# Kernel optimization log

Hardware: AMD Instinct MI355X
Metric: run time of the kernel (lower is better)

Reference implementation:

```python
import jax, jax.numpy as jnp
import numpy as np

DIM = 64
NUM_HEADS = 4
SIGMA_RATIO = 1.0


def setup_inputs() -> dict:
    key = jax.random.key(0)
    ks = jax.random.split(key, 10)
    d = DIM
    s = 0.02
    return {
        "x": jax.random.normal(ks[0], (2, d, 64, 64), dtype=jnp.float32),
        "qkv_w": jax.random.normal(ks[1], (3 * d, d), dtype=jnp.float32) * s,
        "qkv_b": jnp.zeros((3 * d,), dtype=jnp.float32),
        "proj_w": jax.random.normal(ks[2], (d, d), dtype=jnp.float32) * s,
        "proj_b": jnp.zeros((d,), dtype=jnp.float32),
        "g1_w": jax.random.normal(ks[3], (16, 1), dtype=jnp.float32) * 0.5,
        "g1_b": jnp.zeros((16,), dtype=jnp.float32),
        "g2_w": jax.random.normal(ks[4], (NUM_HEADS, 16), dtype=jnp.float32) * 0.5,
        "g2_b": jnp.zeros((NUM_HEADS,), dtype=jnp.float32),
    }


def reference(x, qkv_w, qkv_b, proj_w, proj_b, g1_w, g1_b, g2_w, g2_b):
    B, C, H, W = x.shape
    nh = NUM_HEADS
    hd = C // nh
    N = H * W
    scale = hd ** -0.5

    # edge strength |x[i]-x[i-1]| summed over channels, replicate-padded
    diff_h = jnp.abs(x[:, :, :, 1:] - x[:, :, :, :-1]).sum(axis=1)  # [B,H,W-1]
    diff_v = jnp.abs(x[:, :, 1:, :] - x[:, :, :-1, :]).sum(axis=1)  # [B,H-1,W]
    edge_h = jnp.pad(diff_h, ((0, 0), (0, 0), (0, 1)), mode="edge")
    edge_v = jnp.pad(diff_v, ((0, 0), (0, 1), (0, 0)), mode="edge")
    es = (edge_h + edge_v)[..., None]  # [B,H,W,1]

    # gate MLP: Linear(1,16) -> GELU(exact) -> Linear(16,nh) -> sigmoid
    h1 = jax.nn.gelu(es @ g1_w.T + g1_b, approximate=False)
    gate = jax.nn.sigmoid(h1 @ g2_w.T + g2_b)  # [B,H,W,nh]

    x_seq = x.transpose(0, 2, 3, 1).reshape(B, N, C)
    qkv = (x_seq @ qkv_w.T + qkv_b).reshape(B, N, 3, nh, hd)
    qkv = qkv.transpose(2, 0, 3, 1, 4)  # [3,B,nh,N,hd]
    q, k, v = qkv[0], qkv[1], qkv[2]

    attn = jax.nn.softmax(jnp.einsum("bhnd,bhmd->bhnm", q, k) * scale, axis=-1)

    gate_sender = gate.reshape(B, N, nh).transpose(0, 2, 1)  # [B,nh,N]
    gate_sender = (1.0 - gate_sender * SIGMA_RATIO * 0.1)[..., None]  # [B,nh,N,1]
    attn = attn * gate_sender
    attn = attn / (attn.sum(axis=-1, keepdims=True) + 1e-8)

    out = jnp.einsum("bhnm,bhmd->bnhd", attn, v).reshape(B, N, C)
    out = out @ proj_w.T + proj_b
    return out.reshape(B, H, W, C).transpose(0, 3, 1, 2)
```

## Files before the change

kernel.cpp:

```cpp
#include <hip/hip_runtime.h>
#include <cstdint>


namespace {
constexpr int B  = 2;
constexpr int C  = 64;
constexpr int NH = 4;
constexpr int HD = 16;
constexpr int N  = 4096;
constexpr int MSA = 4;
constexpr int MT  = 256;
constexpr int VROW  = 2 * MT + 16;
constexpr int KSZ   = MT * 32;
constexpr int BUFSZ = KSZ + HD * VROW;

constexpr size_t QKV1     = (size_t)B * NH * N * HD;
constexpr size_t KB_OFF   = QKV1;
constexpr size_t VT_OFF   = 2 * QKV1;
constexpr size_t PO_OFF_U = 3 * QKV1;
constexpr size_t PO_SZ    = (size_t)B * NH * MSA * N * HD;
constexpr size_t PL_OFF_F = (PO_OFF_U + PO_SZ) / 2;
constexpr float QSCALE = 0.36067376022224085f;
}

typedef short bf16x8 __attribute__((ext_vector_type(8)));
typedef float f32x16 __attribute__((ext_vector_type(16)));
typedef int   i32x4  __attribute__((ext_vector_type(4)));

__device__ __forceinline__ unsigned short f2bf(float f) {
  unsigned u = __float_as_uint(f);
  u = (u + 0x7fffu + ((u >> 16) & 1u)) >> 16;
  return (unsigned short)u;
}
__device__ __forceinline__ int cvtpk(float lo, float hi) {
  int r;
  asm("v_cvt_pk_bf16_f32 %0, %1, %2" : "=v"(r) : "v"(lo), "v"(hi));
  return r;
}
__device__ __forceinline__ float fexp2(float x) {
#if __has_builtin(__builtin_amdgcn_exp2f)
  return __builtin_amdgcn_exp2f(x);
#else
  float r;
  asm("v_exp_f32 %0, %1" : "=v"(r) : "v"(x));
  return r;
#endif
}
__device__ __forceinline__ float frcp(float x) {
#if __has_builtin(__builtin_amdgcn_rcpf)
  return __builtin_amdgcn_rcpf(x);
#else
  float r;
  asm("v_rcp_f32 %0, %1" : "=v"(r) : "v"(x));
  return r;
#endif
}
__device__ __forceinline__ void plswap(int a, int b, int h, int& x, int& y) {
#if __has_builtin(__builtin_amdgcn_permlane32_swap)
  (void)h;
  auto r = __builtin_amdgcn_permlane32_swap(a, b, false, false);
  x = r[0]; y = r[1];
#else
  const int ea = __shfl_xor(a, 32), eb = __shfl_xor(b, 32);
  x = h ? eb : a;
  y = h ? b : ea;
#endif
}

__global__ __launch_bounds__(256) void qkv_mfma_kernel(
    const float* __restrict__ x, const float* __restrict__ w,
    const float* __restrict__ bias, unsigned short* __restrict__ qb,
    unsigned short* __restrict__ kb, unsigned short* __restrict__ vtb) {
  __shared__ char wl[64 * 128];
  __shared__ char tl[4 * 2048];
  const int tid = threadIdx.x;
  const int lane = tid & 63, wid = tid >> 6;
  const int l31 = lane & 31, h = lane >> 5;
  const int nw = wid >> 1, jw = wid & 1;
  const int b = blockIdx.y, n0 = blockIdx.x * 64, z = blockIdx.z;

#pragma unroll
  for (int k = 0; k < 8; ++k) {
    const int p = tid + k * 256;
    const int j = p >> 5, c2 = (p & 31) * 2;
    const float2 wv = *(const float2*)(w + ((size_t)z * 64 + j) * 64 + c2);
    *(int*)(wl + j * 128 + ((2 * c2) ^ ((j & 7) << 4))) = cvtpk(wv.x, wv.y);
  }

  const int nA = n0 + nw * 32 + l31;
  bf16x8 af[4];
#pragma unroll
  for (int kk = 0; kk < 4; ++kk) {
    float e[8];
#pragma unroll
    for (int i = 0; i < 8; ++i)
      e[i] = x[((size_t)b * C + kk * 16 + h * 8 + i) * N + nA];
    i32x4 pk = {cvtpk(e[0], e[1]), cvtpk(e[2], e[3]),
                cvtpk(e[4], e[5]), cvtpk(e[6], e[7])};
    af[kk] = __builtin_bit_cast(bf16x8, pk);
  }
  __syncthreads();

  const int j = jw * 32 + l31;
  f32x16 acc = {};
#pragma unroll
  for (int kk = 0; kk < 4; ++kk) {
    bf16x8 bf =
        *(const bf16x8*)(wl + j * 128 + ((kk * 32 + h * 16) ^ ((j & 7) << 4)));
    acc = __builtin_amdgcn_mfma_f32_32x32x16_bf16(af[kk], bf, acc, 0, 0, 0);
  }
  const float bj = bias[z * 64 + j];
  char* myt = tl + wid * 2048;

  if (z < 2) {
    const float sc = (z == 0) ? QSCALE : 1.0f;
#pragma unroll
    for (int r = 0; r < 16; ++r) {
      const int n = (r & 3) + 8 * (r >> 2) + 4 * h;
      *(unsigned short*)(myt + n * 64 + l31 * 2) = f2bf((acc[r] + bj) * sc);
    }
    unsigned short* dst0 = (z == 0) ? qb : kb;
#pragma unroll
    for (int u = 0; u < 2; ++u) {
      const int chunk = lane * 2 + u;
      const int n = chunk >> 2, c = chunk & 3;
      const uint4 vv = *(const uint4*)(myt + n * 64 + c * 16);
      const int jj = jw * 32 + c * 8;
      const int hh = jj >> 4, half = (jj >> 3) & 1;
      *(uint4*)(dst0 + ((size_t)(b * NH + hh) * N + n0 + nw * 32 + n) * HD +
                half * 8) = vv;
    }
  } else {
#pragma unroll
    for (int p = 0; p < 8; ++p) {
      const int r = 2 * p;
      const int n = (r & 3) + 8 * (r >> 2) + 4 * h;
      *(int*)(myt + l31 * 64 + n * 2) = cvtpk(acc[r] + bj, acc[r + 1] + bj);
    }
#pragma unroll
    for (int u = 0; u < 2; ++u) {
      const int chunk = lane * 2 + u;
      const int jj = chunk >> 2, c = chunk & 3;
      const uint4 vv = *(const uint4*)(myt + jj * 64 + c * 16);
      const int vj = jw * 32 + jj;
      const int hh = vj >> 4, hd = vj & 15;
      *(uint4*)(vtb + ((size_t)(b * NH + hh) * HD + hd) * N + n0 + nw * 32 +
                c * 8) = vv;
    }
  }
}

__global__ __launch_bounds__(256) void attn_mfma_kernel(
    const unsigned short* __restrict__ qb, const unsigned short* __restrict__ kb,
    const unsigned short* __restrict__ vtb, unsigned short* __restrict__ part_o,
    float* __restrict__ part_l) {
  __shared__ uint4 ldsq[2 * BUFSZ / 16];
  char* ldsb = (char*)ldsq;
  const int tid  = threadIdx.x;
  const int lane = tid & 63;
  const int wid  = tid >> 6;
  const int l31  = lane & 31;
  const int h    = lane >> 5;
  const int bh = blockIdx.z;
  const int ms = blockIdx.y;
  const int q0 = blockIdx.x * 128 + wid * 32;
  const int m0 = ms * (N / MSA);
  constexpr int nt = (N / MSA) / MT;

  bf16x8 qf;
  {
    const uint4 qv =
        *(const uint4*)(qb + (((size_t)bh * N) + q0 + l31) * HD + h * 8);
    qf = __builtin_bit_cast(bf16x8, qv);
  }

  const unsigned short* kgp = kb + ((size_t)bh * N + m0) * HD;
  const unsigned short* vgp = vtb + (size_t)bh * HD * N + m0;
  const int d0 = tid >> 5, c0 = tid & 31;
  const int d1 = d0 + 8;

  {
    uint4 k0 = *(const uint4*)(kgp + (size_t)tid * 8);
    uint4 k1 = *(const uint4*)(kgp + (size_t)(tid + 256) * 8);
    uint4 v0 = *(const uint4*)(vgp + (size_t)d0 * N + c0 * 8);
    uint4 v1 = *(const uint4*)(vgp + (size_t)d1 * N + c0 * 8);
    *(uint4*)(ldsb + tid * 16) = k0;
    *(uint4*)(ldsb + (tid + 256) * 16) = k1;
    *(uint4*)(ldsb + KSZ + d0 * VROW + c0 * 16) = v0;
    *(uint4*)(ldsb + KSZ + d1 * VROW + c0 * 16) = v1;
  }
  __syncthreads();

  f32x16 acc = {};
  int cur = 0;

  for (int t = 0; t < nt; ++t) {
    uint4 k0{}, k1{}, v0{}, v1{};
    const bool pre = (t + 1 < nt);
    if (pre) {
      const unsigned short* kt = kgp + (size_t)(t + 1) * MT * HD;
      const unsigned short* vt = vgp + (t + 1) * MT;
      k0 = *(const uint4*)(kt + (size_t)tid * 8);
      k1 = *(const uint4*)(kt + (size_t)(tid + 256) * 8);
      v0 = *(const uint4*)(vt + (size_t)d0 * N + c0 * 8);
      v1 = *(const uint4*)(vt + (size_t)d1 * N + c0 * 8);
    }
    const char* kbase = ldsb + cur * BUFSZ;
    const char* vbase = kbase + KSZ;
#pragma unroll
    for (int cc = 0; cc < MT / 32; ++cc) {
      bf16x8 kf = *(const bf16x8*)(kbase + (cc * 32 + l31) * 32 + h * 16);
      f32x16 zv = {};
      f32x16 st = __builtin_amdgcn_mfma_f32_32x32x16_bf16(kf, qf, zv, 0, 0, 0);
      float e[16];
#pragma unroll
      for (int r = 0; r < 16; ++r) e[r] = fexp2(st[r]);
      int dw[8];
#pragma unroll
      for (int jj = 0; jj < 8; ++jj) dw[jj] = cvtpk(e[2 * jj], e[2 * jj + 1]);
      int w0, w1, w2, w3, w4, w5, w6, w7;
      plswap(dw[0], dw[2], h, w0, w2);
      plswap(dw[1], dw[3], h, w1, w3);
      plswap(dw[4], dw[6], h, w4, w6);
      plswap(dw[5], dw[7], h, w5, w7);
      const i32x4 a1 = {w0, w1, w2, w3};
      const i32x4 a2 = {w4, w5, w6, w7};
      bf16x8 vf1, vf2;
      if (l31 < HD) {
        const char* vrow = vbase + l31 * VROW + cc * 64 + h * 16;
        vf1 = *(const bf16x8*)(vrow);
        vf2 = *(const bf16x8*)(vrow + 32);
      } else {
        const int f = (l31 == HD) ? 0x3F803F80 : 0;
        const i32x4 fv = {f, f, f, f};
        vf1 = __builtin_bit_cast(bf16x8, fv);
        vf2 = vf1;
      }
      acc = __builtin_amdgcn_mfma_f32_32x32x16_bf16(
          __builtin_bit_cast(bf16x8, a1), vf1, acc, 0, 0, 0);
      acc = __builtin_amdgcn_mfma_f32_32x32x16_bf16(
          __builtin_bit_cast(bf16x8, a2), vf2, acc, 0, 0, 0);
    }
    if (pre) {
      char* nb = ldsb + (cur ^ 1) * BUFSZ;
      *(uint4*)(nb + tid * 16) = k0;
      *(uint4*)(nb + (tid + 256) * 16) = k1;
      *(uint4*)(nb + KSZ + d0 * VROW + c0 * 16) = v0;
      *(uint4*)(nb + KSZ + d1 * VROW + c0 * 16) = v1;
    }
    __syncthreads();
    cur ^= 1;
  }

  const size_t pbase = ((size_t)bh * MSA + ms) * N + q0;
  if (l31 == HD) {
#pragma unroll
    for (int r = 0; r < 16; ++r)
      part_l[pbase + (r & 3) + 8 * (r >> 2) + 4 * h] = acc[r];
  }
  char* myt = ldsb + wid * 1024;
  if (l31 < HD) {
#pragma unroll
    for (int r = 0; r < 16; ++r) {
      const int q = (r & 3) + 8 * (r >> 2) + 4 * h;
      *(unsigned short*)(myt + q * 32 + l31 * 2) = f2bf(acc[r]);
    }
  }
  __syncthreads();
  const int qr = lane >> 1, half = lane & 1;
  const uint4 vv = *(const uint4*)(myt + qr * 32 + half * 16);
  *(uint4*)(part_o + (pbase + qr) * HD + half * 8) = vv;
}

__global__ __launch_bounds__(128) void proj_mfma_kernel(
    const unsigned short* __restrict__ part_o, const float* __restrict__ part_l,
    const float* __restrict__ pw, const float* __restrict__ pb,
    float* __restrict__ out) {
  __shared__ char al[32 * 128];
  __shared__ char bl[64 * 128];
  __shared__ char tl[2 * 4096];
  __shared__ float linv[128];
  const int tid = threadIdx.x;
  const int lane = tid & 63, wid = tid >> 6;
  const int l31 = lane & 31, h = lane >> 5;
  const int b = blockIdx.y, n0 = blockIdx.x * 32;

  {
    const int hh = tid >> 5, n = tid & 31;
    const size_t base = ((size_t)(b * NH + hh) * MSA) * N + n0 + n;
    float l = 0.f;
#pragma unroll
    for (int ms = 0; ms < MSA; ++ms) l += part_l[base + (size_t)ms * N];
    linv[tid] = frcp(l);
  }
#pragma unroll
  for (int k = 0; k < 16; ++k) {
    const int p = tid + k * 128;
    const int cR = p >> 5, d2 = (p & 31) * 2;
    const float2 wv = *(const float2*)(pw + cR * 64 + d2);
    *(int*)(bl + cR * 128 + ((2 * d2) ^ ((cR & 7) << 4))) = cvtpk(wv.x, wv.y);
  }
  __syncthreads();

#pragma unroll
  for (int u = 0; u < 2; ++u) {
    const int chunk = tid * 2 + u;
    const int hh = chunk >> 6, half = (chunk >> 5) & 1, n = chunk & 31;
    const unsigned short* src =
        part_o + (((size_t)(b * NH + hh) * MSA) * N + n0 + n) * HD + half * 8;
    float s[8] = {0.f, 0.f, 0.f, 0.f, 0.f, 0.f, 0.f, 0.f};
#pragma unroll
    for (int ms = 0; ms < MSA; ++ms) {
      const uint4 v = *(const uint4*)(src + (size_t)ms * N * HD);
      const unsigned uu[4] = {v.x, v.y, v.z, v.w};
#pragma unroll
      for (int q = 0; q < 4; ++q) {
        s[2 * q]     += __uint_as_float(uu[q] << 16);
        s[2 * q + 1] += __uint_as_float(uu[q] & 0xffff0000u);
      }
    }
    const float iv = linv[hh * 32 + n];
    const i32x4 pk = {cvtpk(s[0] * iv, s[1] * iv), cvtpk(s[2] * iv, s[3] * iv),
                      cvtpk(s[4] * iv, s[5] * iv), cvtpk(s[6] * iv, s[7] * iv)};
    const int d = hh * 16 + half * 8;
    *(i32x4*)(al + n * 128 + ((2 * d) ^ ((n & 7) << 4))) = pk;
  }
  __syncthreads();

  bf16x8 af[4];
#pragma unroll
  for (int kk = 0; kk < 4; ++kk)
    af[kk] = *(const bf16x8*)(al + l31 * 128 +
                              ((kk * 32 + h * 16) ^ ((l31 & 7) << 4)));
  const int c = wid * 32 + l31;
  f32x16 acc = {};
#pragma unroll
  for (int kk = 0; kk < 4; ++kk) {
    bf16x8 bf =
        *(const bf16x8*)(bl + c * 128 + ((kk * 32 + h * 16) ^ ((c & 7) << 4)));
    acc = __builtin_amdgcn_mfma_f32_32x32x16_bf16(af[kk], bf, acc, 0, 0, 0);
  }
  const float bc = pb[c];

  char* myt = tl + wid * 4096;
#pragma unroll
  for (int p = 0; p < 8; ++p) {
    const int r = 2 * p;
    const int n = (r & 3) + 8 * (r >> 2) + 4 * h;
    *(float2*)(myt + l31 * 128 + n * 4) =
        make_float2(acc[r] + bc, acc[r + 1] + bc);
  }
  __syncthreads();
#pragma unroll
  for (int u = 0; u < 4; ++u) {
    const int chunk = lane * 4 + u;
    const int cc = chunk >> 3, cq = chunk & 7;
    const float4 vv = *(const float4*)(myt + cc * 128 + cq * 16);
    *(float4*)(out + ((size_t)b * C + wid * 32 + cc) * N + n0 + cq * 4) = vv;
  }
}

extern "C" void kernel_launch(void* const* d_in, const int* in_sizes, int n_in,
                              void* d_out, int out_size, void* d_ws, size_t ws_size,
                              hipStream_t stream) {
  const float* x      = (const float*)d_in[0];
  const float* qkv_w  = (const float*)d_in[1];
  const float* qkv_b  = (const float*)d_in[2];
  const float* proj_w = (const float*)d_in[3];
  const float* proj_b = (const float*)d_in[4];
  unsigned short* qb     = (unsigned short*)d_ws;
  unsigned short* kb     = qb + KB_OFF;
  unsigned short* vtb    = qb + VT_OFF;
  unsigned short* part_o = qb + PO_OFF_U;
  float* part_l = (float*)d_ws + PL_OFF_F;
  float* out = (float*)d_out;

  qkv_mfma_kernel<<<dim3(N / 64, B, 3), 256, 0, stream>>>(
      x, qkv_w, qkv_b, qb, kb, vtb);
  attn_mfma_kernel<<<dim3(N / 128, MSA, B * NH), 256, 0, stream>>>(
      qb, kb, vtb, part_o, part_l);
  proj_mfma_kernel<<<dim3(N / 32, B), 128, 0, stream>>>(
      part_o, part_l, proj_w, proj_b, out);
}
```

Measured before the change: 39.11 us.

## Software-pipeline QK MFMA across chunks and retile K layout for conflict-free LDS

K is now written by the QKV kernel in a chunked layout (32-key blocks split by half of the head dimension), so each lane's LDS read of a K fragment is a contiguous 16-byte row rather than a strided one. The attention loop issues the next chunk's QK MFMA before the exp2/pack/PV work of the current chunk, so the score MFMA latency overlaps with the softmax math. The constant V fragment for the row-sum lanes is hoisted out of the loop, and launch bounds now request 4 blocks per CU. This costs more live registers, and the K producer and consumer must agree exactly on the new layout.

Result: faster. 35.05 us, median of 3 (-10.4%).

```diff
diff --git a/kernel.cpp b/kernel.cpp
--- a/kernel.cpp
+++ b/kernel.cpp
@@ -119,7 +119,6 @@
       const int n = (r & 3) + 8 * (r >> 2) + 4 * h;
       *(unsigned short*)(myt + n * 64 + l31 * 2) = f2bf((acc[r] + bj) * sc);
     }
-    unsigned short* dst0 = (z == 0) ? qb : kb;
 #pragma unroll
     for (int u = 0; u < 2; ++u) {
       const int chunk = lane * 2 + u;
@@ -127,8 +126,14 @@
       const uint4 vv = *(const uint4*)(myt + n * 64 + c * 16);
       const int jj = jw * 32 + c * 8;
       const int hh = jj >> 4, half = (jj >> 3) & 1;
-      *(uint4*)(dst0 + ((size_t)(b * NH + hh) * N + n0 + nw * 32 + n) * HD +
-                half * 8) = vv;
+      const int bh = b * NH + hh;
+      if (z == 0) {
+        *(uint4*)(qb + ((size_t)bh * N + n0 + nw * 32 + n) * HD + half * 8) = vv;
+      } else {
+        const size_t ck = (size_t)bh * 8192 +
+                          (size_t)((n0 >> 5) + nw) * 64 + half * 32 + n;
+        *(uint4*)(kb + ck * 8) = vv;
+      }
     }
   } else {
 #pragma unroll
@@ -150,7 +155,7 @@
   }
 }
 
-__global__ __launch_bounds__(256) void attn_mfma_kernel(
+__global__ __launch_bounds__(256, 4) void attn_mfma_kernel(
     const unsigned short* __restrict__ qb, const unsigned short* __restrict__ kb,
     const unsigned short* __restrict__ vtb, unsigned short* __restrict__ part_o,
     float* __restrict__ part_l) {
@@ -173,8 +178,7 @@
         *(const uint4*)(qb + (((size_t)bh * N) + q0 + l31) * HD + h * 8);
     qf = __builtin_bit_cast(bf16x8, qv);
   }
-
-  const unsigned short* kgp = kb + ((size_t)bh * N + m0) * HD;
+  const unsigned short* kgp = kb + ((size_t)bh * 8192 + (m0 >> 5) * 64) * 8;
   const unsigned short* vgp = vtb + (size_t)bh * HD * N + m0;
   const int d0 = tid >> 5, c0 = tid & 31;
   const int d1 = d0 + 8;
@@ -191,14 +195,17 @@
   }
   __syncthreads();
 
+  const int onef = (l31 == HD) ? 0x3F803F80 : 0;
+  const i32x4 onev = {onef, onef, onef, onef};
+  const bf16x8 vcst = __builtin_bit_cast(bf16x8, onev);
+
   f32x16 acc = {};
   int cur = 0;
-
   for (int t = 0; t < nt; ++t) {
     uint4 k0{}, k1{}, v0{}, v1{};
     const bool pre = (t + 1 < nt);
     if (pre) {
-      const unsigned short* kt = kgp + (size_t)(t + 1) * MT * HD;
+      const unsigned short* kt = kgp + (size_t)(t + 1) * 512 * 8;
       const unsigned short* vt = vgp + (t + 1) * MT;
       k0 = *(const uint4*)(kt + (size_t)tid * 8);
       k1 = *(const uint4*)(kt + (size_t)(tid + 256) * 8);
@@ -207,17 +214,32 @@
     }
     const char* kbase = ldsb + cur * BUFSZ;
     const char* vbase = kbase + KSZ;
+
+    bf16x8 kf = *(const bf16x8*)(kbase + (h * 32 + l31) * 16);
+    f32x16 zv = {};
+    f32x16 stn = __builtin_amdgcn_mfma_f32_32x32x16_bf16(kf, qf, zv, 0, 0, 0);
+
 #pragma unroll
     for (int cc = 0; cc < MT / 32; ++cc) {
-      bf16x8 kf = *(const bf16x8*)(kbase + (cc * 32 + l31) * 32 + h * 16);
-      f32x16 zv = {};
-      f32x16 st = __builtin_amdgcn_mfma_f32_32x32x16_bf16(kf, qf, zv, 0, 0, 0);
-      float e[16];
-#pragma unroll
-      for (int r = 0; r < 16; ++r) e[r] = fexp2(st[r]);
+      const f32x16 st = stn;
+      if (cc + 1 < MT / 32) {
+        bf16x8 kf2 =
+            *(const bf16x8*)(kbase + ((cc + 1) * 64 + h * 32 + l31) * 16);
+        stn = __builtin_amdgcn_mfma_f32_32x32x16_bf16(kf2, qf, zv, 0, 0, 0);
+      }
+      bf16x8 vf1, vf2;
+      if (l31 < HD) {
+        const char* vrow = vbase + l31 * VROW + cc * 64 + h * 16;
+        vf1 = *(const bf16x8*)(vrow);
+        vf2 = *(const bf16x8*)(vrow + 32);
+      } else {
+        vf1 = vcst;
+        vf2 = vcst;
+      }
       int dw[8];
 #pragma unroll
-      for (int jj = 0; jj < 8; ++jj) dw[jj] = cvtpk(e[2 * jj], e[2 * jj + 1]);
+      for (int jj = 0; jj < 8; ++jj)
+        dw[jj] = cvtpk(fexp2(st[2 * jj]), fexp2(st[2 * jj + 1]));
       int w0, w1, w2, w3, w4, w5, w6, w7;
       plswap(dw[0], dw[2], h, w0, w2);
       plswap(dw[1], dw[3], h, w1, w3);
@@ -225,17 +247,6 @@
       plswap(dw[5], dw[7], h, w5, w7);
       const i32x4 a1 = {w0, w1, w2, w3};
       const i32x4 a2 = {w4, w5, w6, w7};
-      bf16x8 vf1, vf2;
-      if (l31 < HD) {
-        const char* vrow = vbase + l31 * VROW + cc * 64 + h * 16;
-        vf1 = *(const bf16x8*)(vrow);
-        vf2 = *(const bf16x8*)(vrow + 32);
-      } else {
-        const int f = (l31 == HD) ? 0x3F803F80 : 0;
-        const i32x4 fv = {f, f, f, f};
-        vf1 = __builtin_bit_cast(bf16x8, fv);
-        vf2 = vf1;
-      }
       acc = __builtin_amdgcn_mfma_f32_32x32x16_bf16(
           __builtin_bit_cast(bf16x8, a1), vf1, acc, 0, 0, 0);
       acc = __builtin_amdgcn_mfma_f32_32x32x16_bf16(
```
